# Kernel tuning notes

Hardware: AMD Instinct MI355X
Metric: run time of the kernel (lower is better)

## Reference

```python
import jax, jax.numpy as jnp
import numpy as np

B, C, H, W = 8, 384, 32, 32
NUM_HEADS = 8
HEAD_DIM = C // NUM_HEADS
HIDDEN = max(32, C // 2)


def setup_inputs() -> dict:
    key = jax.random.key(0)
    ks = jax.random.split(key, 6)
    s = lambda fan_in: 1.0 / np.sqrt(fan_in)
    return {
        "x": jax.random.normal(ks[0], (B, C, H, W), dtype=jnp.float32),
        "qkv_w": jax.random.normal(ks[1], (C, 3 * C), dtype=jnp.float32) * s(C),
        "qkv_b": jnp.zeros((3 * C,), dtype=jnp.float32),
        "proj_w": jax.random.normal(ks[2], (C, C), dtype=jnp.float32) * s(C),
        "proj_b": jnp.zeros((C,), dtype=jnp.float32),
        "mlp_w1": jax.random.normal(ks[3], (2, HIDDEN), dtype=jnp.float32) * s(2),
        "mlp_b1": jnp.zeros((HIDDEN,), dtype=jnp.float32),
        "mlp_w2": jax.random.normal(ks[4], (HIDDEN, NUM_HEADS), dtype=jnp.float32) * s(HIDDEN),
        "mlp_b2": jnp.zeros((NUM_HEADS,), dtype=jnp.float32),
    }


def _relative_bias(h, w, mlp_w1, mlp_b1, mlp_w2, mlp_b2):
    ch = jnp.arange(h, dtype=jnp.float32)
    cw = jnp.arange(w, dtype=jnp.float32)
    coords = jnp.stack(jnp.meshgrid(ch, cw, indexing="ij"), axis=-1).reshape(-1, 2)  # [N,2]
    rel = coords[:, None, :] - coords[None, :, :]  # [N,N,2]
    denom = jnp.array([max(h - 1, 1), max(w - 1, 1)], dtype=jnp.float32)
    rel = rel / denom
    hidden = jax.nn.gelu(rel @ mlp_w1 + mlp_b1, approximate=False)
    bias = hidden @ mlp_w2 + mlp_b2  # [N,N,heads]
    return jnp.transpose(bias, (2, 0, 1))  # [heads,N,N]


def reference(x, qkv_w, qkv_b, proj_w, proj_b, mlp_w1, mlp_b1, mlp_w2, mlp_b2):
    b, c, h, w = x.shape
    n = h * w
    tokens = x.reshape(b, c, n).transpose(0, 2, 1)  # [B,N,C]
    qkv = (tokens @ qkv_w + qkv_b).reshape(b, n, 3, NUM_HEADS, HEAD_DIM)
    qkv = jnp.transpose(qkv, (2, 0, 3, 1, 4))  # [3,B,h,N,d]
    q, k, v = qkv[0], qkv[1], qkv[2]
    scale = HEAD_DIM ** -0.5
    attn = jnp.einsum("bhnd,bhmd->bhnm", q * scale, k)
    attn = attn + _relative_bias(h, w, mlp_w1, mlp_b1, mlp_w2, mlp_b2)[None]
    attn = jax.nn.softmax(attn, axis=-1)
    out = jnp.einsum("bhnm,bhmd->bhnd", attn, v)
    out = out.transpose(0, 2, 1, 3).reshape(b, n, c)
    out = out @ proj_w + proj_b
    return out.transpose(0, 2, 1).reshape(b, c, h, w)
```

## Files before the change

### kernel.cpp

```cpp
#include <hip/hip_runtime.h>
#include <hip/hip_bf16.h>
#include <math.h>

#define BB 8
#define CC 384
#define NT 1024
#define NHEAD 8
#define HD 48
#define HIDDEN 192
#define THREEC 1152

typedef short short8 __attribute__((ext_vector_type(8)));
typedef short short4v __attribute__((ext_vector_type(4)));
typedef float f32x4 __attribute__((ext_vector_type(4)));
typedef unsigned int uint2v __attribute__((ext_vector_type(2)));
typedef unsigned int uint4v __attribute__((ext_vector_type(4)));

static __device__ __forceinline__ short bf16bits(float v) {
  __hip_bfloat16 h = __float2bfloat16(v);
  return *(short*)&h;
}
static __device__ __forceinline__ unsigned pk2(float a, float b) {
  return __builtin_amdgcn_perm(__float_as_uint(b) + 0x8000u,
                               __float_as_uint(a) + 0x8000u, 0x07060302u);
}
static __device__ __forceinline__ unsigned cvtpk(float lo, float hi) {
  unsigned r;
  asm("v_cvt_pk_bf16_f32 %0, %1, %2" : "=v"(r) : "v"(lo), "v"(hi));
  return r;
}
static __device__ __forceinline__ void lds_dma16(const void* g, void* l) {
  __builtin_amdgcn_global_load_lds((const __attribute__((address_space(1))) unsigned*)g,
                                   (__attribute__((address_space(3))) unsigned*)l, 16, 0, 0);
}
static __device__ __forceinline__ void pl16swap(unsigned& a, unsigned& b) {
  asm("v_permlane16_swap_b32 %0, %1" : "+v"(a), "+v"(b));
}
static __device__ __forceinline__ float exp2_raw(float x) {
  float r;
  asm("v_exp_f32 %0, %1" : "=v"(r) : "v"(x));
  return r;
}

__global__ __launch_bounds__(256) void k_prep(
    const float* __restrict__ x, const float* __restrict__ qkv_w,
    const float* __restrict__ proj_w,
    const float* __restrict__ w1, const float* __restrict__ b1,
    const float* __restrict__ w2, const float* __restrict__ b2,
    __hip_bfloat16* __restrict__ xt, __hip_bfloat16* __restrict__ wtq,
    __hip_bfloat16* __restrict__ wtp, float* __restrict__ tab) {
  const int bid = blockIdx.x;
  const int tid = threadIdx.x;
  if (bid >= 3648) {
    int g = (bid - 3648) * 256 + tid;
    int p = g >> 3, jc = g & 7;
    if (p >= 63 * 63) return;
    float rh = (float)(p / 63 - 31) * (1.0f / 31.0f);
    float rw = (float)(p % 63 - 31) * (1.0f / 31.0f);
    float acc[8] = {0.f, 0.f, 0.f, 0.f, 0.f, 0.f, 0.f, 0.f};
    const int j0 = jc * 24;
#pragma unroll 4
    for (int j = j0; j < j0 + 24; j++) {
      float pre = fmaf(rh, w1[j], fmaf(rw, w1[HIDDEN + j], b1[j]));
      float gl = 0.5f * pre * (1.0f + erff(pre * 0.70710678118654752f));
#pragma unroll
      for (int h = 0; h < 8; h++) acc[h] = fmaf(gl, w2[j * 8 + h], acc[h]);
    }
#pragma unroll
    for (int msk = 1; msk <= 4; msk <<= 1)
#pragma unroll
      for (int h = 0; h < 8; h++) acc[h] += __shfl_xor(acc[h], msk);
    if (jc == 0) {
#pragma unroll
      for (int h = 0; h < 8; h++)
        tab[h * 3969 + p] = (acc[h] + b2[h]) * 1.4426950408889634f;
    }
    return;
  }
  const float* src;
  __hip_bfloat16* dst;
  int R, C, r0, c0;
  if (bid < 3072) {
    int zi = bid / 384, rem = bid % 384;
    R = 384; C = 1024;
    r0 = (rem / 32) * 32; c0 = (rem % 32) * 32;
    src = x + (size_t)zi * R * C;
    dst = xt + (size_t)zi * R * C;
  } else if (bid < 3504) {
    int i = bid - 3072;
    R = 384; C = 1152;
    r0 = (i / 36) * 32; c0 = (i % 36) * 32;
    src = qkv_w; dst = wtq;
  } else {
    int i = bid - 3504;
    R = 384; C = 384;
    r0 = (i / 12) * 32; c0 = (i % 12) * 32;
    src = proj_w; dst = wtp;
  }
  __shared__ float t[32][33];
#pragma unroll
  for (int e = 0; e < 4; e++) {
    int i = tid + e * 256;
    int r = i >> 5, c = i & 31;
    t[r][c] = src[(size_t)(r0 + r) * C + c0 + c];
  }
  __syncthreads();
#pragma unroll
  for (int e = 0; e < 4; e++) {
    int i = tid + e * 256;
    int c = i >> 5, r = i & 31;
    dst[(size_t)(c0 + c) * R + r0 + r] = __float2bfloat16(t[r][c]);
  }
}

__global__ __launch_bounds__(256) void k_qkv_mfma(
    const __hip_bfloat16* __restrict__ xt,
    const __hip_bfloat16* __restrict__ wtq,
    const float* __restrict__ qkv_b,
    __hip_bfloat16* __restrict__ Qb,
    __hip_bfloat16* __restrict__ Kb,
    __hip_bfloat16* __restrict__ Vt)
{
  __shared__ __align__(16) char smem[17408];
  short* As = (short*)smem;
  short* Bs = (short*)(smem + 8192);
  float* Vf = (float*)smem;
  const int n0 = blockIdx.x * 64;
  const int m0 = blockIdx.y * 64;
  const int tid = threadIdx.x;
  const int wv = tid >> 6, lane = tid & 63, quad = lane >> 4, lq = lane & 15;
  const int lrow = lane >> 3;
  const int gsw = ((lane & 7) ^ lrow) * 8;
  const int sw0 = (quad ^ (lq & 7)) * 8;
  const int sw1 = sw0 ^ 32;
  f32x4 acc[4];
#pragma unroll
  for (int nt = 0; nt < 4; nt++) acc[nt] = (f32x4){0.f, 0.f, 0.f, 0.f};
  for (int kk = 0; kk < CC; kk += 64) {
    __syncthreads();
    for (int c = wv; c < 16; c += 4) {
      if (c < 8)
        lds_dma16((const short*)xt + (size_t)(m0 + c * 8 + lrow) * 384 + kk + gsw,
                  smem + c * 1024);
      else
        lds_dma16((const short*)wtq + (size_t)(n0 + (c - 8) * 8 + lrow) * 384 + kk + gsw,
                  smem + 8192 + (c - 8) * 1024);
    }
    __syncthreads();
    short8 a0 = *(const short8*)(As + (wv * 16 + lq) * 64 + sw0);
    short8 a1 = *(const short8*)(As + (wv * 16 + lq) * 64 + sw1);
#pragma unroll
    for (int nt = 0; nt < 4; nt++) {
      acc[nt] = __builtin_amdgcn_mfma_f32_16x16x32_bf16(
          a0, *(const short8*)(Bs + (nt * 16 + lq) * 64 + sw0), acc[nt], 0, 0, 0);
      acc[nt] = __builtin_amdgcn_mfma_f32_16x16x32_bf16(
          a1, *(const short8*)(Bs + (nt * 16 + lq) * 64 + sw1), acc[nt], 0, 0, 0);
    }
  }
  __syncthreads();
  const float qscale = 0.14433756729740643f * 1.4426950408889634f;
  const float sc = (n0 < 384) ? qscale : 1.0f;
#pragma unroll
  for (int nt = 0; nt < 4; nt++) {
    float bias = qkv_b[n0 + nt * 16 + lq];
#pragma unroll
    for (int r = 0; r < 4; r++)
      Vf[(nt * 16 + lq) * 68 + wv * 16 + quad * 4 + r] = (acc[nt][r] + bias) * sc;
  }
  __syncthreads();
  if (n0 >= 768) {
    int ch = tid & 63, grp = tid >> 6;
    int cg = n0 - 768 + ch;
    int head = cg / 48, d = cg - head * 48;
    int b = m0 >> 10;
    int n = (m0 & 1023) + grp * 16;
    const float* src = Vf + ch * 68 + grp * 16;
    short o16[16];
#pragma unroll
    for (int k = 0; k < 16; k++) o16[k] = bf16bits(src[k]);
    short* dst = (short*)Vt + ((size_t)(b * 8 + head) * 48 + d) * 1024 + n;
    *(short8*)dst = *(short8*)o16;
    *(short8*)(dst + 8) = *(short8*)(o16 + 8);
  } else {
    const int which = n0 >= 384;
    short* Out = which ? (short*)Kb : (short*)Qb;
    int n_l = tid & 63, seg = tid >> 6;
    int rr0 = (n0 - which * 384) + seg * 16;
    int head = rr0 / 48, d0 = rr0 - head * 48;
    int b = m0 >> 10;
    int n_g = (m0 & 1023) + n_l;
    const float* src = Vf + (seg * 16) * 68 + n_l;
    short o16[16];
#pragma unroll
    for (int k = 0; k < 16; k++) o16[k] = bf16bits(src[k * 68]);
    short* dst = Out + (((size_t)(b * 8 + head) << 10) + n_g) * 64 + d0;
    *(short8*)dst = *(short8*)o16;
    *(short8*)(dst + 8) = *(short8*)(o16 + 8);
    if (d0 == 0) {
      short8 z = (short8){0, 0, 0, 0, 0, 0, 0, 0};
      *(short8*)(dst + 48) = z;
      *(short8*)(dst + 56) = z;
    }
  }
}

#define K0_OFF 0
#define V0_OFF 16384
#define TR_OFF 28672
#define SMEM_SZ 32768
__global__ __launch_bounds__(512, 4) void k_flash(
    const __hip_bfloat16* __restrict__ Qb, const __hip_bfloat16* __restrict__ Kb,
    const __hip_bfloat16* __restrict__ Vt, const float* __restrict__ tab,
    __hip_bfloat16* __restrict__ ATb)
{
  __shared__ __align__(16) char smem[SMEM_SZ];
  float* Os = (float*)smem;

  const int tid = threadIdx.x;
  const int wv = tid >> 6, lane = tid & 63, quad = lane >> 4, lq = lane & 15;
  const int bh = blockIdx.x;
  const int q0 = blockIdx.y * 128;
  const int b = bh >> 3, h = bh & 7;
  const int inr0 = q0 >> 5;

  const int nrow = q0 + wv * 16 + lq;
  const int jnr = nrow & 31;
  const int rloc = (nrow >> 5) - inr0 + 1;
  const int tbase = rloc * 63 + jnr + 31 - 4 * quad;

  short8 qf0, qf1;
  {
    const short* qp = (const short*)Qb + ((size_t)(bh << 10) + nrow) * 64;
    qf0 = *(const short8*)(qp + quad * 8);
    qf1 = *(const short8*)(qp + 32 + quad * 8);
  }
  short8 onesv;
#pragma unroll
  for (int j = 0; j < 8; j++) onesv[j] = (short)0x3F80;

  f32x4 O[4];
#pragma unroll
  for (int dt = 0; dt < 4; dt++) O[dt] = (f32x4){0.f, 0.f, 0.f, 0.f};

  const short* kgp = (const short*)Kb + ((size_t)(bh << 10)) * 64;
  const short* vgp = (const short*)Vt + (size_t)bh * 48 * 1024;
  const float* tabg = tab + h * 3969;
  const int lrow = lane >> 3;
  const int gsw = ((lane & 7) ^ lrow) * 8;
  const int sw0 = (quad ^ (lq & 7)) * 8;
  const int sw1 = sw0 ^ 32;
  const int vq = ((quad & 1) << 1) | (quad >> 1);
  const int swv0 = (vq ^ (lq & 7)) * 8;
  const int swv1 = swv0 ^ 32;

  const char* ksrc = (const char*)kgp + (((size_t)(wv * 8 + lrow) * 64 + gsw) << 1);
  const int kd = K0_OFF + wv * 1024;
  const char* s2src;
  int s2stride, s2d, s2dalt;
  if (wv < 6) {
    s2src = (const char*)vgp + (((size_t)(wv * 8 + lrow) * 1024 + gsw) << 1);
    s2stride = 128;
    s2d = V0_OFF + wv * 1024;
    s2dalt = 6144;
  } else {
    s2src = (const char*)(tabg + (inr0 + 30) * 63 + lane * 4 + (wv == 7 ? 256 : 0));
    s2stride = -504;
    s2d = TR_OFF + (wv == 7 ? 1024 : 0);
    s2dalt = 2048;
  }
  lds_dma16(ksrc, smem + kd);
  lds_dma16(s2src, smem + s2d);

  for (int it = 0; it < 16; it++) {
    const int buf = it & 1;
    __syncthreads();
    if (it < 15) {
      const int nbuf = buf ^ 1;
      ksrc += 8192;
      s2src += s2stride;
      lds_dma16(ksrc, smem + kd + nbuf * 8192);
      lds_dma16(s2src, smem + s2d + nbuf * s2dalt);
    }
    const short* Kl = (const short*)(smem + K0_OFF + buf * 8192);
    const short* Vl = (const short*)(smem + V0_OFF + buf * 6144);
    const float* Tl = (const float*)(smem + TR_OFF + buf * 2048);

    float s[4][4];
    __builtin_amdgcn_s_setprio(1);
#pragma unroll
    for (int nt = 0; nt < 4; nt++) {
      const float* tn = Tl + tbase - (nt >= 2 ? 63 : 0) - (nt & 1) * 16;
      f32x4 c;
      c[0] = tn[0]; c[1] = tn[-1]; c[2] = tn[-2]; c[3] = tn[-3];
      c = __builtin_amdgcn_mfma_f32_16x16x32_bf16(
          *(const short8*)(Kl + (nt * 16 + lq) * 64 + sw0), qf0, c, 0, 0, 0);
      c = __builtin_amdgcn_mfma_f32_16x16x32_bf16(
          *(const short8*)(Kl + (nt * 16 + lq) * 64 + sw1), qf1, c, 0, 0, 0);
#pragma unroll
      for (int r = 0; r < 4; r++) s[nt][r] = c[r];
    }
    __builtin_amdgcn_s_setprio(0);
#pragma unroll
    for (int nt = 0; nt < 4; nt++)
#pragma unroll
      for (int r = 0; r < 4; r++) s[nt][r] = exp2_raw(s[nt][r]);
    uint4v p0, p1;
    {
      unsigned a, bb_;
      a = cvtpk(s[0][0], s[0][1]); bb_ = cvtpk(s[1][0], s[1][1]);
      pl16swap(a, bb_); p0[0] = a; p0[2] = bb_;
      a = cvtpk(s[0][2], s[0][3]); bb_ = cvtpk(s[1][2], s[1][3]);
      pl16swap(a, bb_); p0[1] = a; p0[3] = bb_;
      a = cvtpk(s[2][0], s[2][1]); bb_ = cvtpk(s[3][0], s[3][1]);
      pl16swap(a, bb_); p1[0] = a; p1[2] = bb_;
      a = cvtpk(s[2][2], s[2][3]); bb_ = cvtpk(s[3][2], s[3][3]);
      pl16swap(a, bb_); p1[1] = a; p1[3] = bb_;
    }
    short8 pf0 = *(short8*)&p0;
    short8 pf1 = *(short8*)&p1;
    __builtin_amdgcn_s_setprio(1);
#pragma unroll
    for (int dt = 0; dt < 3; dt++)
      O[dt] = __builtin_amdgcn_mfma_f32_16x16x32_bf16(
          *(const short8*)(Vl + (dt * 16 + lq) * 64 + swv0), pf0, O[dt], 0, 0, 0);
    O[3] = __builtin_amdgcn_mfma_f32_16x16x32_bf16(onesv, pf0, O[3], 0, 0, 0);
#pragma unroll
    for (int dt = 0; dt < 3; dt++)
      O[dt] = __builtin_amdgcn_mfma_f32_16x16x32_bf16(
          *(const short8*)(Vl + (dt * 16 + lq) * 64 + swv1), pf1, O[dt], 0, 0, 0);
    O[3] = __builtin_amdgcn_mfma_f32_16x16x32_bf16(onesv, pf1, O[3], 0, 0, 0);
    __builtin_amdgcn_s_setprio(0);
  }
  float inv = 1.0f / O[3][0];
  __syncthreads();
#pragma unroll
  for (int dt = 0; dt < 3; dt++)
#pragma unroll
    for (int r = 0; r < 4; r++)
      Os[(wv * 16 + lq) * 52 + dt * 16 + quad * 4 + r] = O[dt][r] * inv;
  __syncthreads();
  {
    int row = tid >> 2, cg = (tid & 3) * 12;
    const float* src = Os + row * 52 + cg;
    short outp[12];
#pragma unroll
    for (int k = 0; k < 12; k++) outp[k] = bf16bits(src[k]);
    short* dst = (short*)ATb + ((size_t)(b << 10) + q0 + row) * 384 + h * 48 + cg;
    *(short4v*)dst = *(short4v*)outp;
    *(short4v*)(dst + 4) = *(short4v*)(outp + 4);
    *(short4v*)(dst + 8) = *(short4v*)(outp + 8);
  }
}

__global__ __launch_bounds__(256) void k_proj_mfma(
    const __hip_bfloat16* __restrict__ ATb,
    const __hip_bfloat16* __restrict__ wtp,
    const float* __restrict__ pb, float* __restrict__ out) {
  __shared__ __align__(16) char smem[16384];
  short* As = (short*)smem;
  short* Bs = (short*)(smem + 8192);
  const int c0 = blockIdx.x * 64;
  const int n0 = blockIdx.y * 64;
  const int b = blockIdx.z;
  const int tid = threadIdx.x;
  const int wv = tid >> 6, lane = tid & 63, quad = lane >> 4, lq = lane & 15;
  const int lrow = lane >> 3;
  const int gsw = ((lane & 7) ^ lrow) * 8;
  const int sw0 = (quad ^ (lq & 7)) * 8;
  const int sw1 = sw0 ^ 32;
  f32x4 acc[4];
#pragma unroll
  for (int nt = 0; nt < 4; nt++) acc[nt] = (f32x4){0.f, 0.f, 0.f, 0.f};
  for (int kk = 0; kk < CC; kk += 64) {
    __syncthreads();
    for (int c = wv; c < 16; c += 4) {
      if (c < 8)
        lds_dma16((const short*)wtp + (size_t)(c0 + c * 8 + lrow) * 384 + kk + gsw,
                  smem + c * 1024);
      else
        lds_dma16((const short*)ATb + ((size_t)(b << 10) + n0 + (c - 8) * 8 + lrow) * 384 + kk + gsw,
                  smem + 8192 + (c - 8) * 1024);
    }
    __syncthreads();
    short8 a0 = *(const short8*)(As + (wv * 16 + lq) * 64 + sw0);
    short8 a1 = *(const short8*)(As + (wv * 16 + lq) * 64 + sw1);
#pragma unroll
    for (int nt = 0; nt < 4; nt++) {
      acc[nt] = __builtin_amdgcn_mfma_f32_16x16x32_bf16(
          a0, *(const short8*)(Bs + (nt * 16 + lq) * 64 + sw0), acc[nt], 0, 0, 0);
      acc[nt] = __builtin_amdgcn_mfma_f32_16x16x32_bf16(
          a1, *(const short8*)(Bs + (nt * 16 + lq) * 64 + sw1), acc[nt], 0, 0, 0);
    }
  }
#pragma unroll
  for (int nt = 0; nt < 4; nt++) {
    int n = n0 + nt * 16 + lq;
#pragma unroll
    for (int r = 0; r < 4; r++) {
      int c = c0 + wv * 16 + quad * 4 + r;
      out[((size_t)b * 384 + c) * 1024 + n] = acc[nt][r] + pb[c];
    }
  }
}

extern "C" void kernel_launch(void* const* d_in, const int* in_sizes, int n_in,
                              void* d_out, int out_size, void* d_ws, size_t ws_size,
                              hipStream_t stream) {
  const float* x = (const float*)d_in[0];
  const float* qkv_w = (const float*)d_in[1];
  const float* qkv_b = (const float*)d_in[2];
  const float* proj_w = (const float*)d_in[3];
  const float* proj_b = (const float*)d_in[4];
  const float* w1 = (const float*)d_in[5];
  const float* b1 = (const float*)d_in[6];
  const float* w2 = (const float*)d_in[7];
  const float* b2 = (const float*)d_in[8];
  float* out = (float*)d_out;

  char* w = (char*)d_ws;
  __hip_bfloat16* xt = (__hip_bfloat16*)w;   w += (size_t)8192 * 384 * 2;
  __hip_bfloat16* wtq = (__hip_bfloat16*)w;  w += (size_t)1152 * 384 * 2;
  __hip_bfloat16* wtp = (__hip_bfloat16*)w;  w += (size_t)384 * 384 * 2;
  __hip_bfloat16* Qb = (__hip_bfloat16*)w;   w += (size_t)64 * 1024 * 64 * 2;
  __hip_bfloat16* Kb = (__hip_bfloat16*)w;   w += (size_t)64 * 1024 * 64 * 2;
  __hip_bfloat16* Vt = (__hip_bfloat16*)w;   w += (size_t)64 * 48 * 1024 * 2;
  __hip_bfloat16* ATb = (__hip_bfloat16*)w;  w += (size_t)8192 * 384 * 2;
  float* tab = (float*)w;                    w += (size_t)8 * 3969 * 4 + 1024;

  k_prep<<<dim3(3773), dim3(256), 0, stream>>>(x, qkv_w, proj_w, w1, b1, w2, b2,
                                               xt, wtq, wtp, tab);
  k_qkv_mfma<<<dim3(18, 128), dim3(256), 0, stream>>>(xt, wtq, qkv_b, Qb, Kb, Vt);
  k_flash<<<dim3(64, 8), dim3(512), 0, stream>>>(Qb, Kb, Vt, tab, ATb);
  k_proj_mfma<<<dim3(6, 16, 8), dim3(256), 0, stream>>>(ATb, wtp, proj_b, out);
}
```

Measured before the change: 154.7 us.

## Process two query tiles per wave in flash kernel with 256-thread blocks

Halves the flash-attention block to 4 waves, each wave now handling 32 query rows as two 16-row MFMA tiles that share the K and V fragments read from LDS. This halves the LDS fragment reads per unit of work and doubles MFMA work per wave, giving more instruction-level parallelism. Each wave now issues four DMA loads per iteration instead of two. The cost is higher register pressure from two accumulator sets and fewer waves per block for latency hiding. The unused pk2 helper is removed.

```diff
diff --git a/kernel.cpp b/kernel.cpp
--- a/kernel.cpp
+++ b/kernel.cpp
@@ -19,10 +19,6 @@
 static __device__ __forceinline__ short bf16bits(float v) {
   __hip_bfloat16 h = __float2bfloat16(v);
   return *(short*)&h;
-}
-static __device__ __forceinline__ unsigned pk2(float a, float b) {
-  return __builtin_amdgcn_perm(__float_as_uint(b) + 0x8000u,
-                               __float_as_uint(a) + 0x8000u, 0x07060302u);
 }
 static __device__ __forceinline__ unsigned cvtpk(float lo, float hi) {
   unsigned r;
@@ -208,7 +204,7 @@
 #define V0_OFF 16384
 #define TR_OFF 28672
 #define SMEM_SZ 32768
-__global__ __launch_bounds__(512, 4) void k_flash(
+__global__ __launch_bounds__(256, 2) void k_flash(
     const __hip_bfloat16* __restrict__ Qb, const __hip_bfloat16* __restrict__ Kb,
     const __hip_bfloat16* __restrict__ Vt, const float* __restrict__ tab,
     __hip_bfloat16* __restrict__ ATb)
@@ -223,24 +219,28 @@
   const int b = bh >> 3, h = bh & 7;
   const int inr0 = q0 >> 5;
 
-  const int nrow = q0 + wv * 16 + lq;
-  const int jnr = nrow & 31;
-  const int rloc = (nrow >> 5) - inr0 + 1;
-  const int tbase = rloc * 63 + jnr + 31 - 4 * quad;
-
-  short8 qf0, qf1;
+  const int nrowA = q0 + wv * 32 + lq;
+  const int tbaseA = (wv + 1) * 63 + lq + 31 - 4 * quad;
+  const int tbaseB = tbaseA + 16;
+
+  short8 qfA0, qfA1, qfB0, qfB1;
   {
-    const short* qp = (const short*)Qb + ((size_t)(bh << 10) + nrow) * 64;
-    qf0 = *(const short8*)(qp + quad * 8);
-    qf1 = *(const short8*)(qp + 32 + quad * 8);
+    const short* qp = (const short*)Qb + ((size_t)(bh << 10) + nrowA) * 64;
+    qfA0 = *(const short8*)(qp + quad * 8);
+    qfA1 = *(const short8*)(qp + 32 + quad * 8);
+    qfB0 = *(const short8*)(qp + 1024 + quad * 8);
+    qfB1 = *(const short8*)(qp + 1024 + 32 + quad * 8);
   }
   short8 onesv;
 #pragma unroll
   for (int j = 0; j < 8; j++) onesv[j] = (short)0x3F80;
 
-  f32x4 O[4];
-#pragma unroll
-  for (int dt = 0; dt < 4; dt++) O[dt] = (f32x4){0.f, 0.f, 0.f, 0.f};
+  f32x4 OA[4], OB[4];
+#pragma unroll
+  for (int dt = 0; dt < 4; dt++) {
+    OA[dt] = (f32x4){0.f, 0.f, 0.f, 0.f};
+    OB[dt] = (f32x4){0.f, 0.f, 0.f, 0.f};
+  }
 
   const short* kgp = (const short*)Kb + ((size_t)(bh << 10)) * 64;
   const short* vgp = (const short*)Vt + (size_t)bh * 48 * 1024;
@@ -253,102 +253,137 @@
   const int swv0 = (vq ^ (lq & 7)) * 8;
   const int swv1 = swv0 ^ 32;
 
-  const char* ksrc = (const char*)kgp + (((size_t)(wv * 8 + lrow) * 64 + gsw) << 1);
-  const int kd = K0_OFF + wv * 1024;
-  const char* s2src;
-  int s2stride, s2d, s2dalt;
-  if (wv < 6) {
-    s2src = (const char*)vgp + (((size_t)(wv * 8 + lrow) * 1024 + gsw) << 1);
-    s2stride = 128;
-    s2d = V0_OFF + wv * 1024;
-    s2dalt = 6144;
+  const char* kAsrc = (const char*)kgp + (((size_t)(wv * 8 + lrow) * 64 + gsw) << 1);
+  const char* kBsrc = (const char*)kgp + (((size_t)((wv + 4) * 8 + lrow) * 64 + gsw) << 1);
+  const int kAd = K0_OFF + wv * 1024;
+  const int kBd = K0_OFF + (wv + 4) * 1024;
+  const char* vsrc = (const char*)vgp + (((size_t)(wv * 8 + lrow) * 1024 + gsw) << 1);
+  const int vd = V0_OFF + wv * 1024;
+  const char* u4src;
+  int u4stride, u4d, u4alt;
+  if (wv < 2) {
+    u4src = (const char*)vgp + (((size_t)((wv + 4) * 8 + lrow) * 1024 + gsw) << 1);
+    u4stride = 128;
+    u4d = V0_OFF + (wv + 4) * 1024;
+    u4alt = 6144;
   } else {
-    s2src = (const char*)(tabg + (inr0 + 30) * 63 + lane * 4 + (wv == 7 ? 256 : 0));
-    s2stride = -504;
-    s2d = TR_OFF + (wv == 7 ? 1024 : 0);
-    s2dalt = 2048;
-  }
-  lds_dma16(ksrc, smem + kd);
-  lds_dma16(s2src, smem + s2d);
+    u4src = (const char*)(tabg + (inr0 + 30) * 63 + lane * 4 + (wv == 3 ? 256 : 0));
+    u4stride = -504;
+    u4d = TR_OFF + (wv == 3 ? 1024 : 0);
+    u4alt = 2048;
+  }
+  lds_dma16(kAsrc, smem + kAd);
+  lds_dma16(kBsrc, smem + kBd);
+  lds_dma16(vsrc, smem + vd);
+  lds_dma16(u4src, smem + u4d);
 
   for (int it = 0; it < 16; it++) {
     const int buf = it & 1;
     __syncthreads();
     if (it < 15) {
       const int nbuf = buf ^ 1;
-      ksrc += 8192;
-      s2src += s2stride;
-      lds_dma16(ksrc, smem + kd + nbuf * 8192);
-      lds_dma16(s2src, smem + s2d + nbuf * s2dalt);
+      kAsrc += 8192; kBsrc += 8192; vsrc += 128; u4src += u4stride;
+      lds_dma16(kAsrc, smem + kAd + nbuf * 8192);
+      lds_dma16(kBsrc, smem + kBd + nbuf * 8192);
+      lds_dma16(vsrc, smem + vd + nbuf * 6144);
+      lds_dma16(u4src, smem + u4d + nbuf * u4alt);
     }
     const short* Kl = (const short*)(smem + K0_OFF + buf * 8192);
     const short* Vl = (const short*)(smem + V0_OFF + buf * 6144);
     const float* Tl = (const float*)(smem + TR_OFF + buf * 2048);
 
-    float s[4][4];
+    float sA[4][4], sB[4][4];
     __builtin_amdgcn_s_setprio(1);
 #pragma unroll
     for (int nt = 0; nt < 4; nt++) {
-      const float* tn = Tl + tbase - (nt >= 2 ? 63 : 0) - (nt & 1) * 16;
+      short8 kf0 = *(const short8*)(Kl + (nt * 16 + lq) * 64 + sw0);
+      short8 kf1 = *(const short8*)(Kl + (nt * 16 + lq) * 64 + sw1);
+      const float* tnA = Tl + tbaseA - (nt >= 2 ? 63 : 0) - (nt & 1) * 16;
       f32x4 c;
-      c[0] = tn[0]; c[1] = tn[-1]; c[2] = tn[-2]; c[3] = tn[-3];
-      c = __builtin_amdgcn_mfma_f32_16x16x32_bf16(
-          *(const short8*)(Kl + (nt * 16 + lq) * 64 + sw0), qf0, c, 0, 0, 0);
-      c = __builtin_amdgcn_mfma_f32_16x16x32_bf16(
-          *(const short8*)(Kl + (nt * 16 + lq) * 64 + sw1), qf1, c, 0, 0, 0);
-#pragma unroll
-      for (int r = 0; r < 4; r++) s[nt][r] = c[r];
+      c[0] = tnA[0]; c[1] = tnA[-1]; c[2] = tnA[-2]; c[3] = tnA[-3];
+      c = __builtin_amdgcn_mfma_f32_16x16x32_bf16(kf0, qfA0, c, 0, 0, 0);
+      c = __builtin_amdgcn_mfma_f32_16x16x32_bf16(kf1, qfA1, c, 0, 0, 0);
+#pragma unroll
+      for (int r = 0; r < 4; r++) sA[nt][r] = c[r];
+      const float* tnB = tnA + 16;
+      f32x4 d;
+      d[0] = tnB[0]; d[1] = tnB[-1]; d[2] = tnB[-2]; d[3] = tnB[-3];
+      d = __builtin_amdgcn_mfma_f32_16x16x32_bf16(kf0, qfB0, d, 0, 0, 0);
+      d = __builtin_amdgcn_mfma_f32_16x16x32_bf16(kf1, qfB1, d, 0, 0, 0);
+#pragma unroll
+      for (int r = 0; r < 4; r++) sB[nt][r] = d[r];
     }
     __builtin_amdgcn_s_setprio(0);
 #pragma unroll
     for (int nt = 0; nt < 4; nt++)
 #pragma unroll
-      for (int r = 0; r < 4; r++) s[nt][r] = exp2_raw(s[nt][r]);
-    uint4v p0, p1;
+      for (int r = 0; r < 4; r++) {
+        sA[nt][r] = exp2_raw(sA[nt][r]);
+        sB[nt][r] = exp2_raw(sB[nt][r]);
+      }
+    uint4v pA0, pA1, pB0, pB1;
     {
       unsigned a, bb_;
-      a = cvtpk(s[0][0], s[0][1]); bb_ = cvtpk(s[1][0], s[1][1]);
-      pl16swap(a, bb_); p0[0] = a; p0[2] = bb_;
-      a = cvtpk(s[0][2], s[0][3]); bb_ = cvtpk(s[1][2], s[1][3]);
-      pl16swap(a, bb_); p0[1] = a; p0[3] = bb_;
-      a = cvtpk(s[2][0], s[2][1]); bb_ = cvtpk(s[3][0], s[3][1]);
-      pl16swap(a, bb_); p1[0] = a; p1[2] = bb_;
-      a = cvtpk(s[2][2], s[2][3]); bb_ = cvtpk(s[3][2], s[3][3]);
-      pl16swap(a, bb_); p1[1] = a; p1[3] = bb_;
-    }
-    short8 pf0 = *(short8*)&p0;
-    short8 pf1 = *(short8*)&p1;
+      a = cvtpk(sA[0][0], sA[0][1]); bb_ = cvtpk(sA[1][0], sA[1][1]);
+      pl16swap(a, bb_); pA0[0] = a; pA0[2] = bb_;
+      a = cvtpk(sA[0][2], sA[0][3]); bb_ = cvtpk(sA[1][2], sA[1][3]);
+      pl16swap(a, bb_); pA0[1] = a; pA0[3] = bb_;
+      a = cvtpk(sA[2][0], sA[2][1]); bb_ = cvtpk(sA[3][0], sA[3][1]);
+      pl16swap(a, bb_); pA1[0] = a; pA1[2] = bb_;
+      a = cvtpk(sA[2][2], sA[2][3]); bb_ = cvtpk(sA[3][2], sA[3][3]);
+      pl16swap(a, bb_); pA1[1] = a; pA1[3] = bb_;
+      a = cvtpk(sB[0][0], sB[0][1]); bb_ = cvtpk(sB[1][0], sB[1][1]);
+      pl16swap(a, bb_); pB0[0] = a; pB0[2] = bb_;
+      a = cvtpk(sB[0][2], sB[0][3]); bb_ = cvtpk(sB[1][2], sB[1][3]);
+      pl16swap(a, bb_); pB0[1] = a; pB0[3] = bb_;
+      a = cvtpk(sB[2][0], sB[2][1]); bb_ = cvtpk(sB[3][0], sB[3][1]);
+      pl16swap(a, bb_); pB1[0] = a; pB1[2] = bb_;
+      a = cvtpk(sB[2][2], sB[2][3]); bb_ = cvtpk(sB[3][2], sB[3][3]);
+      pl16swap(a, bb_); pB1[1] = a; pB1[3] = bb_;
+    }
+    short8 pfA0 = *(short8*)&pA0;
+    short8 pfA1 = *(short8*)&pA1;
+    short8 pfB0 = *(short8*)&pB0;
+    short8 pfB1 = *(short8*)&pB1;
     __builtin_amdgcn_s_setprio(1);
 #pragma unroll
-    for (int dt = 0; dt < 3; dt++)
-      O[dt] = __builtin_amdgcn_mfma_f32_16x16x32_bf16(
-          *(const short8*)(Vl + (dt * 16 + lq) * 64 + swv0), pf0, O[dt], 0, 0, 0);
-    O[3] = __builtin_amdgcn_mfma_f32_16x16x32_bf16(onesv, pf0, O[3], 0, 0, 0);
-#pragma unroll
-    for (int dt = 0; dt < 3; dt++)
-      O[dt] = __builtin_amdgcn_mfma_f32_16x16x32_bf16(
-          *(const short8*)(Vl + (dt * 16 + lq) * 64 + swv1), pf1, O[dt], 0, 0, 0);
-    O[3] = __builtin_amdgcn_mfma_f32_16x16x32_bf16(onesv, pf1, O[3], 0, 0, 0);
+    for (int dt = 0; dt < 3; dt++) {
+      short8 vf = *(const short8*)(Vl + (dt * 16 + lq) * 64 + swv0);
+      OA[dt] = __builtin_amdgcn_mfma_f32_16x16x32_bf16(vf, pfA0, OA[dt], 0, 0, 0);
+      OB[dt] = __builtin_amdgcn_mfma_f32_16x16x32_bf16(vf, pfB0, OB[dt], 0, 0, 0);
+    }
+    OA[3] = __builtin_amdgcn_mfma_f32_16x16x32_bf16(onesv, pfA0, OA[3], 0, 0, 0);
+    OB[3] = __builtin_amdgcn_mfma_f32_16x16x32_bf16(onesv, pfB0, OB[3], 0, 0, 0);
+#pragma unroll
+    for (int dt = 0; dt < 3; dt++) {
+      short8 vf = *(const short8*)(Vl + (dt * 16 + lq) * 64 + swv1);
+      OA[dt] = __builtin_amdgcn_mfma_f32_16x16x32_bf16(vf, pfA1, OA[dt], 0, 0, 0);
+      OB[dt] = __builtin_amdgcn_mfma_f32_16x16x32_bf16(vf, pfB1, OB[dt], 0, 0, 0);
+    }
+    OA[3] = __builtin_amdgcn_mfma_f32_16x16x32_bf16(onesv, pfA1, OA[3], 0, 0, 0);
+    OB[3] = __builtin_amdgcn_mfma_f32_16x16x32_bf16(onesv, pfB1, OB[3], 0, 0, 0);
     __builtin_amdgcn_s_setprio(0);
   }
-  float inv = 1.0f / O[3][0];
+  float invA = 1.0f / OA[3][0];
+  float invB = 1.0f / OB[3][0];
   __syncthreads();
 #pragma unroll
   for (int dt = 0; dt < 3; dt++)
 #pragma unroll
-    for (int r = 0; r < 4; r++)
-      Os[(wv * 16 + lq) * 52 + dt * 16 + quad * 4 + r] = O[dt][r] * inv;
+    for (int r = 0; r < 4; r++) {
+      Os[(wv * 32 + lq) * 52 + dt * 16 + quad * 4 + r] = OA[dt][r] * invA;
+      Os[(wv * 32 + 16 + lq) * 52 + dt * 16 + quad * 4 + r] = OB[dt][r] * invB;
+    }
   __syncthreads();
   {
-    int row = tid >> 2, cg = (tid & 3) * 12;
+    int row = tid >> 1, cg = (tid & 1) * 24;
     const float* src = Os + row * 52 + cg;
-    short outp[12];
-#pragma unroll
-    for (int k = 0; k < 12; k++) outp[k] = bf16bits(src[k]);
+    short outp[24];
+#pragma unroll
+    for (int k = 0; k < 24; k++) outp[k] = bf16bits(src[k]);
     short* dst = (short*)ATb + ((size_t)(b << 10) + q0 + row) * 384 + h * 48 + cg;
-    *(short4v*)dst = *(short4v*)outp;
-    *(short4v*)(dst + 4) = *(short4v*)(outp + 4);
-    *(short4v*)(dst + 8) = *(short4v*)(outp + 8);
+#pragma unroll
+    for (int g = 0; g < 6; g++) *(short4v*)(dst + g * 4) = *(short4v*)(outp + g * 4);
   }
 }
 
@@ -430,6 +465,6 @@
   k_prep<<<dim3(3773), dim3(256), 0, stream>>>(x, qkv_w, proj_w, w1, b1, w2, b2,
                                                xt, wtq, wtp, tab);
   k_qkv_mfma<<<dim3(18, 128), dim3(256), 0, stream>>>(xt, wtq, qkv_b, Qb, Kb, Vt);
-  k_flash<<<dim3(64, 8), dim3(512), 0, stream>>>(Qb, Kb, Vt, tab, ATb);
+  k_flash<<<dim3(64, 8), dim3(256), 0, stream>>>(Qb, Kb, Vt, tab, ATb);
   k_proj_mfma<<<dim3(6, 16, 8), dim3(256), 0, stream>>>(ATb, wtp, proj_b, out);
 }
```

New measurement: 151.0 us. -2.4%, faster.
